# Kernel optimization log

Hardware: AMD Instinct MI355X
Metric: run time of the kernel (lower is better)

Reference implementation:

```python
import jax, jax.numpy as jnp
import numpy as np

N = 100000
E = 1600000
C = 32          # in_channels
H = 256         # hidden_size


def setup_inputs() -> dict:
    key = jax.random.key(0)
    ks = jax.random.split(key, 16)
    s = 1.0 / np.sqrt(C)
    inp = {
        "state": jax.random.normal(ks[0], (N, C), dtype=jnp.float32),
        "edge_index": jax.random.randint(ks[1], (2, E), 0, N, dtype=jnp.int64),
        # GCNConv params (conv3 reused for layers 4 and 5, matching the source)
        "convW1": jax.random.normal(ks[2], (C, C), dtype=jnp.float32) * s,
        "convb1": jnp.zeros((C,), jnp.float32),
        "convW2": jax.random.normal(ks[3], (C, C), dtype=jnp.float32) * s,
        "convb2": jnp.zeros((C,), jnp.float32),
        "convW3": jax.random.normal(ks[4], (C, C), dtype=jnp.float32) * s,
        "convb3": jnp.zeros((C,), jnp.float32),
        "linW1": jax.random.normal(ks[5], (6 * C, H), dtype=jnp.float32) / np.sqrt(6 * C),
        "linb1": jnp.zeros((H,), jnp.float32),
        "linW2": jax.random.normal(ks[6], (H, H), dtype=jnp.float32) / np.sqrt(H),
        "linb2": jnp.zeros((H,), jnp.float32),
        "linW3": jax.random.normal(ks[7], (H, 1), dtype=jnp.float32) / np.sqrt(H),
        "linb3": jnp.zeros((1,), jnp.float32),
    }
    return inp


def _gcn(x, W, b, src, dst, norm):
    # PyG GCNConv: x' = scatter_add( norm * (xW)[src] -> dst ) + b
    xw = x @ W                                  # [N, C]
    msg = norm[:, None] * xw[src]               # [E+N, C] gather
    agg = jax.ops.segment_sum(msg, dst, num_segments=x.shape[0])
    return agg + b


def reference(state, edge_index, convW1, convb1, convW2, convb2, convW3, convb3,
              linW1, linb1, linW2, linb2, linW3, linb3):
    n = state.shape[0]
    loops = jnp.arange(n, dtype=edge_index.dtype)
    src = jnp.concatenate([edge_index[0], loops])   # add self loops
    dst = jnp.concatenate([edge_index[1], loops])
    deg = jax.ops.segment_sum(jnp.ones_like(dst, dtype=state.dtype), dst, num_segments=n)
    dinv = jnp.where(deg > 0, jax.lax.rsqrt(deg), 0.0)
    norm = dinv[src] * dinv[dst]                    # symmetric normalization

    out1 = jax.nn.relu(_gcn(state, convW1, convb1, src, dst, norm))
    out2 = jax.nn.relu(_gcn(out1, convW2, convb2, src, dst, norm))
    out3 = jax.nn.relu(_gcn(out2, convW3, convb3, src, dst, norm))
    out4 = jax.nn.relu(_gcn(out3, convW3, convb3, src, dst, norm))  # conv3 reused (as in source)
    out5 = jax.nn.relu(_gcn(out4, convW3, convb3, src, dst, norm))  # conv3 reused (as in source)

    x = jnp.concatenate([out1, out2, out3, out4, out5, state], axis=-1)  # [N, 6C]
    x = jax.nn.leaky_relu(x @ linW1 + linb1, negative_slope=0.01)
    x = jax.nn.leaky_relu(x @ linW2 + linb2, negative_slope=0.01)
    x = jax.nn.softplus(x @ linW3 + linb3)
    concentration = jnp.squeeze(x, -1)              # [N]
    # deterministic=True path
    action = concentration / (concentration.sum(axis=-1, keepdims=True) + 1e-20)
    return action
```

## Files before the change

### kernel.cpp

```cpp
#include <hip/hip_runtime.h>
#include <hip/hip_bf16.h>
#include <hip/hip_fp16.h>

#define CDIV(a,b) (((a)+(b)-1)/(b))

typedef float f32x4 __attribute__((ext_vector_type(4)));
typedef int   i32x4 __attribute__((ext_vector_type(4)));
typedef unsigned int u32x2 __attribute__((ext_vector_type(2)));

__device__ __forceinline__ void mfma16(f32x4& d, i32x4 a, i32x4 b) {
  asm("v_mfma_f32_16x16x32_bf16 %0, %1, %2, %0" : "+v"(d) : "v"(a), "v"(b));
}

__device__ __forceinline__ unsigned short bf16r(float x) {
  return __builtin_bit_cast(unsigned short, __float2bfloat16(x));
}
__device__ __forceinline__ float bf16f(unsigned short u) {
  unsigned int w_ = (unsigned int)u << 16;
  return __builtin_bit_cast(float, w_);
}


__global__ __launch_bounds__(256) void k_count(const int* __restrict__ dst,
                                               int* __restrict__ cnt, int E) {
  int e = blockIdx.x * blockDim.x + threadIdx.x;
  if (e < E) atomicAdd(&cnt[dst[e]], 1);
}

__global__ __launch_bounds__(256) void k_scan1(const int* __restrict__ cnt,
                                               int* __restrict__ rowptr,
                                               int* __restrict__ blockSums, int N) {
  __shared__ int sdata[256];
  const int t = threadIdx.x;
  const int base = blockIdx.x * 1024;
  int v[4]; int local = 0;
#pragma unroll
  for (int i = 0; i < 4; i++) {
    int idx = base + t * 4 + i;
    v[i] = (idx < N) ? cnt[idx] : 0;
    local += v[i];
  }
  sdata[t] = local;
  __syncthreads();
  for (int off = 1; off < 256; off <<= 1) {
    int x = (t >= off) ? sdata[t - off] : 0;
    __syncthreads();
    sdata[t] += x;
    __syncthreads();
  }
  if (t == 255) blockSums[blockIdx.x] = sdata[255];
  int run = sdata[t] - local;
#pragma unroll
  for (int i = 0; i < 4; i++) {
    int idx = base + t * 4 + i;
    if (idx < N) rowptr[idx] = run;
    run += v[i];
  }
}

__global__ __launch_bounds__(256) void k_scan2(int* blockSums, int NB) {
  __shared__ int sdata[256];
  int t = threadIdx.x;
  int v = (t < NB) ? blockSums[t] : 0;
  sdata[t] = v;
  __syncthreads();
  for (int off = 1; off < 256; off <<= 1) {
    int x = (t >= off) ? sdata[t - off] : 0;
    __syncthreads();
    sdata[t] += x;
    __syncthreads();
  }
  if (t < NB) blockSums[t] = sdata[t] - v;
}

__global__ __launch_bounds__(256) void k_scan3(int* __restrict__ rowptr,
                                               const int* __restrict__ blockSums,
                                               int N, int E) {
  int idx = blockIdx.x * blockDim.x + threadIdx.x;
  if (idx < N) rowptr[idx] += blockSums[idx >> 10];
  if (idx == 0) rowptr[N] = E;
}

__global__ __launch_bounds__(256) void k_fill(const int* __restrict__ src,
                                              const int* __restrict__ dst,
                                              const int* __restrict__ rowptr,
                                              int* __restrict__ cursor,
                                              int* __restrict__ colidx, int E) {
  int e = blockIdx.x * blockDim.x + threadIdx.x;
  if (e < E) {
    int d = dst[e];
    int pos = rowptr[d] + atomicAdd(&cursor[d], 1);
    colidx[pos] = src[e];
  }
}

__global__ __launch_bounds__(256) void k_dinv(const int* __restrict__ cnt,
                                              float* __restrict__ dinv, int N) {
  int i = blockIdx.x * blockDim.x + threadIdx.x;
  if (i < N) dinv[i] = rsqrtf((float)cnt[i] + 1.0f);
}

__global__ __launch_bounds__(256) void k_xw(const float* __restrict__ x,
                                            const float* __restrict__ W,
                                            const float* __restrict__ dinv,
                                            unsigned short* __restrict__ y, int N) {
  __shared__ float Ws[1024];
  int t = threadIdx.x;
#pragma unroll
  for (int i = 0; i < 4; i++) Ws[t + i * 256] = W[t + i * 256];
  __syncthreads();
  int gid = blockIdx.x * blockDim.x + t;
  int n = gid >> 4, c = (gid & 15) * 2;
  if (n < N) {
    const float4* xr4 = (const float4*)(x + (size_t)n * 32);
    float a0 = 0.f, a1 = 0.f;
#pragma unroll
    for (int k4 = 0; k4 < 8; k4++) {
      float4 xv = xr4[k4];
      int k = k4 * 4;
      a0 = fmaf(xv.x, Ws[(k + 0) * 32 + c], a0); a1 = fmaf(xv.x, Ws[(k + 0) * 32 + c + 1], a1);
      a0 = fmaf(xv.y, Ws[(k + 1) * 32 + c], a0); a1 = fmaf(xv.y, Ws[(k + 1) * 32 + c + 1], a1);
      a0 = fmaf(xv.z, Ws[(k + 2) * 32 + c], a0); a1 = fmaf(xv.z, Ws[(k + 2) * 32 + c + 1], a1);
      a0 = fmaf(xv.w, Ws[(k + 3) * 32 + c], a0); a1 = fmaf(xv.w, Ws[(k + 3) * 32 + c + 1], a1);
    }
    float dn = dinv[n];
    __half2 h = __floats2half2_rn(a0 * dn, a1 * dn);
    *(__half2*)&y[(size_t)gid * 2] = h;
  }
}

__device__ __forceinline__ void acc8(float* acc, uint4 v) {
  float2 f;
  f = __half22float2(__builtin_bit_cast(__half2, v.x)); acc[0] += f.x; acc[1] += f.y;
  f = __half22float2(__builtin_bit_cast(__half2, v.y)); acc[2] += f.x; acc[3] += f.y;
  f = __half22float2(__builtin_bit_cast(__half2, v.z)); acc[4] += f.x; acc[5] += f.y;
  f = __half22float2(__builtin_bit_cast(__half2, v.w)); acc[6] += f.x; acc[7] += f.y;
}

__global__ __launch_bounds__(256) void k_agg(const unsigned short* __restrict__ y,
                                             const int* __restrict__ rowptr,
                                             const int* __restrict__ colidx,
                                             const float* __restrict__ dinv,
                                             const float* __restrict__ b,
                                             float* __restrict__ out, int N) {
  int t = threadIdx.x;
  int q = t & 3;
  int n = blockIdx.x * 64 + (t >> 2);
  if (n >= N) return;
  const uint4* yrow = (const uint4*)y;
  float acc[8];
  {
    uint4 v = yrow[(size_t)n * 4 + q];
    float2 f;
    f = __half22float2(__builtin_bit_cast(__half2, v.x)); acc[0] = f.x; acc[1] = f.y;
    f = __half22float2(__builtin_bit_cast(__half2, v.y)); acc[2] = f.x; acc[3] = f.y;
    f = __half22float2(__builtin_bit_cast(__half2, v.z)); acc[4] = f.x; acc[5] = f.y;
    f = __half22float2(__builtin_bit_cast(__half2, v.w)); acc[6] = f.x; acc[7] = f.y;
  }
  int beg = rowptr[n], end = rowptr[n + 1];
  int j = beg;
  for (; j + 16 <= end; j += 16) {
    uint4 v[16];
#pragma unroll
    for (int u = 0; u < 16; u++) v[u] = yrow[(size_t)colidx[j + u] * 4 + q];
#pragma unroll
    for (int u = 0; u < 16; u++) acc8(acc, v[u]);
  }
  for (; j + 8 <= end; j += 8) {
    uint4 v[8];
#pragma unroll
    for (int u = 0; u < 8; u++) v[u] = yrow[(size_t)colidx[j + u] * 4 + q];
#pragma unroll
    for (int u = 0; u < 8; u++) acc8(acc, v[u]);
  }
  for (; j + 4 <= end; j += 4) {
    uint4 v[4];
#pragma unroll
    for (int u = 0; u < 4; u++) v[u] = yrow[(size_t)colidx[j + u] * 4 + q];
#pragma unroll
    for (int u = 0; u < 4; u++) acc8(acc, v[u]);
  }
  for (; j < end; j++) {
    uint4 v = yrow[(size_t)colidx[j] * 4 + q];
    acc8(acc, v);
  }
  float dn = dinv[n];
  int cb = q * 8;
  float4 r0, r1;
  r0.x = fmaxf(fmaf(dn, acc[0], b[cb + 0]), 0.f);
  r0.y = fmaxf(fmaf(dn, acc[1], b[cb + 1]), 0.f);
  r0.z = fmaxf(fmaf(dn, acc[2], b[cb + 2]), 0.f);
  r0.w = fmaxf(fmaf(dn, acc[3], b[cb + 3]), 0.f);
  r1.x = fmaxf(fmaf(dn, acc[4], b[cb + 4]), 0.f);
  r1.y = fmaxf(fmaf(dn, acc[5], b[cb + 5]), 0.f);
  r1.z = fmaxf(fmaf(dn, acc[6], b[cb + 6]), 0.f);
  r1.w = fmaxf(fmaf(dn, acc[7], b[cb + 7]), 0.f);
  ((float4*)out)[(size_t)n * 8 + q * 2 + 0] = r0;
  ((float4*)out)[(size_t)n * 8 + q * 2 + 1] = r1;
}

__global__ __launch_bounds__(256) void k_prepw(const float* __restrict__ W1,
                                               const float* __restrict__ W2,
                                               unsigned short* __restrict__ Wt1h,
                                               unsigned short* __restrict__ Wt1l,
                                               unsigned short* __restrict__ Wt2h,
                                               unsigned short* __restrict__ Wt2l) {
  int o = blockIdx.x * blockDim.x + threadIdx.x;
  if (o < 256 * 192) {
    int col = o / 192, k = o % 192;
    float v = W1[k * 256 + col];
    unsigned short h = bf16r(v);
    Wt1h[o] = h;
    Wt1l[o] = bf16r(v - bf16f(h));
  } else if (o < 256 * 192 + 256 * 256) {
    int o2 = o - 256 * 192;
    int col = o2 / 256, k = o2 % 256;
    float v = W2[k * 256 + col];
    unsigned short h = bf16r(v);
    Wt2h[o2] = h;
    Wt2l[o2] = bf16r(v - bf16f(h));
  }
}

__device__ __forceinline__ float softplusf(float x) {
  return fmaxf(x, 0.f) + log1pf(expf(-fabsf(x)));
}

#define XS_STRIDE 200
#define H1_STRIDE 264
#define MNODES 64

__global__ __launch_bounds__(512, 4) void k_mlp_mfma(
    const float* __restrict__ o1, const float* __restrict__ o2,
    const float* __restrict__ o3, const float* __restrict__ o4,
    const float* __restrict__ o5, const float* __restrict__ st,
    const unsigned short* __restrict__ Wt1h, const unsigned short* __restrict__ Wt1l,
    const float* __restrict__ b1,
    const unsigned short* __restrict__ Wt2h, const unsigned short* __restrict__ Wt2l,
    const float* __restrict__ b2,
    const float* __restrict__ W3, const float* __restrict__ b3,
    float* __restrict__ conc, int N) {
  __shared__ unsigned short smem[2 * MNODES * XS_STRIDE];
  __shared__ float red[8][MNODES];
  unsigned short* xsh = smem;
  unsigned short* xsl = smem + MNODES * XS_STRIDE;
  unsigned short* h1h = smem;

  const int t = threadIdx.x;
  const int w = t >> 6;
  const int l = t & 63;
  const int l15 = l & 15, lq = l >> 4;
  const int nodeBase = blockIdx.x * MNODES;

  const float* srcs[6] = {o1, o2, o3, o4, o5, st};
  for (int i = t; i < MNODES * 96; i += 512) {
    int n = i / 96, cp = (i % 96) * 2;
    int gn = nodeBase + n;
    unsigned int pkh = 0, pkl = 0;
    if (gn < N) {
      const float* s = srcs[cp >> 5] + (size_t)gn * 32 + (cp & 31);
      float2 v = *(const float2*)s;
      unsigned short h0 = bf16r(v.x), h1_ = bf16r(v.y);
      unsigned short l0 = bf16r(v.x - bf16f(h0)), l1 = bf16r(v.y - bf16f(h1_));
      pkh = ((unsigned)h1_ << 16) | h0;
      pkl = ((unsigned)l1 << 16) | l0;
    }
    *(unsigned int*)&xsh[n * XS_STRIDE + cp] = pkh;
    *(unsigned int*)&xsl[n * XS_STRIDE + cp] = pkl;
  }
  __syncthreads();

  const int ocBase = w * 32;

  f32x4 acc[2][4];
#pragma unroll
  for (int rt = 0; rt < 2; rt++)
#pragma unroll
    for (int nt = 0; nt < 4; nt++) acc[rt][nt] = (f32x4)0.f;

  for (int kt = 0; kt < 6; kt++) {
    i32x4 ah[2], al[2];
#pragma unroll
    for (int rt = 0; rt < 2; rt++) {
      size_t aoff = (size_t)(ocBase + rt * 16 + l15) * 192 + kt * 32 + lq * 8;
      ah[rt] = *(const i32x4*)&Wt1h[aoff];
      al[rt] = *(const i32x4*)&Wt1l[aoff];
    }
#pragma unroll
    for (int nt = 0; nt < 4; nt++) {
      int boff = (nt * 16 + l15) * XS_STRIDE + kt * 32 + lq * 8;
      i32x4 bh = *(const i32x4*)&xsh[boff];
      i32x4 bl = *(const i32x4*)&xsl[boff];
#pragma unroll
      for (int rt = 0; rt < 2; rt++) mfma16(acc[rt][nt], ah[rt], bh);
#pragma unroll
      for (int rt = 0; rt < 2; rt++) mfma16(acc[rt][nt], al[rt], bh);
#pragma unroll
      for (int rt = 0; rt < 2; rt++) mfma16(acc[rt][nt], ah[rt], bl);
    }
  }
  __syncthreads();

#pragma unroll
  for (int rt = 0; rt < 2; rt++) {
    const int oc0 = ocBase + rt * 16 + lq * 4;
    float bb0 = b1[oc0], bb1 = b1[oc0 + 1], bb2 = b1[oc0 + 2], bb3 = b1[oc0 + 3];
#pragma unroll
    for (int nt = 0; nt < 4; nt++) {
      float v0 = acc[rt][nt][0] + bb0; v0 = (v0 > 0.f) ? v0 : 0.01f * v0;
      float v1 = acc[rt][nt][1] + bb1; v1 = (v1 > 0.f) ? v1 : 0.01f * v1;
      float v2 = acc[rt][nt][2] + bb2; v2 = (v2 > 0.f) ? v2 : 0.01f * v2;
      float v3 = acc[rt][nt][3] + bb3; v3 = (v3 > 0.f) ? v3 : 0.01f * v3;
      u32x2 pkh;
      pkh[0] = ((unsigned)bf16r(v1) << 16) | bf16r(v0);
      pkh[1] = ((unsigned)bf16r(v3) << 16) | bf16r(v2);
      int row = nt * 16 + l15;
      *(u32x2*)&h1h[row * H1_STRIDE + oc0] = pkh;
    }
  }
  __syncthreads();

  f32x4 acc2[2][4];
#pragma unroll
  for (int rt = 0; rt < 2; rt++)
#pragma unroll
    for (int nt = 0; nt < 4; nt++) acc2[rt][nt] = (f32x4)0.f;

  for (int kt = 0; kt < 8; kt++) {
    i32x4 ah[2], al[2];
#pragma unroll
    for (int rt = 0; rt < 2; rt++) {
      size_t aoff = (size_t)(ocBase + rt * 16 + l15) * 256 + kt * 32 + lq * 8;
      ah[rt] = *(const i32x4*)&Wt2h[aoff];
      al[rt] = *(const i32x4*)&Wt2l[aoff];
    }
#pragma unroll
    for (int nt = 0; nt < 4; nt++) {
      int boff = (nt * 16 + l15) * H1_STRIDE + kt * 32 + lq * 8;
      i32x4 bh = *(const i32x4*)&h1h[boff];
#pragma unroll
      for (int rt = 0; rt < 2; rt++) mfma16(acc2[rt][nt], ah[rt], bh);
#pragma unroll
      for (int rt = 0; rt < 2; rt++) mfma16(acc2[rt][nt], al[rt], bh);
    }
  }

#pragma unroll
  for (int nt = 0; nt < 4; nt++) {
    float p = 0.f;
#pragma unroll
    for (int rt = 0; rt < 2; rt++) {
      const int oc0 = ocBase + rt * 16 + lq * 4;
#pragma unroll
      for (int j = 0; j < 4; j++) {
        float v = acc2[rt][nt][j] + b2[oc0 + j];
        v = (v > 0.f) ? v : 0.01f * v;
        p = fmaf(v, W3[oc0 + j], p);
      }
    }
    p += __shfl_xor(p, 16, 64);
    p += __shfl_xor(p, 32, 64);
    if (lq == 0) red[w][nt * 16 + l15] = p;
  }
  __syncthreads();

  if (t < MNODES) {
    int gn = nodeBase + t;
    if (gn < N) {
      float s = red[0][t] + red[1][t] + red[2][t] + red[3][t]
              + red[4][t] + red[5][t] + red[6][t] + red[7][t] + b3[0];
      conc[gn] = softplusf(s);
    }
  }
}

__global__ __launch_bounds__(256) void k_redsum(const float* __restrict__ conc,
                                                float* __restrict__ total, int N) {
  float s = 0.f;
  for (int i = blockIdx.x * blockDim.x + threadIdx.x; i < N; i += gridDim.x * blockDim.x)
    s += conc[i];
#pragma unroll
  for (int off = 32; off > 0; off >>= 1) s += __shfl_down(s, off, 64);
  __shared__ float ws_[4];
  if ((threadIdx.x & 63) == 0) ws_[threadIdx.x >> 6] = s;
  __syncthreads();
  if (threadIdx.x == 0) atomicAdd(total, ws_[0] + ws_[1] + ws_[2] + ws_[3]);
}

__global__ __launch_bounds__(256) void k_div(const float* __restrict__ conc,
                                             const float* __restrict__ total,
                                             float* __restrict__ out, int N) {
  int i = blockIdx.x * blockDim.x + threadIdx.x;
  if (i < N) out[i] = conc[i] / (total[0] + 1e-20f);
}

extern "C" void kernel_launch(void* const* d_in, const int* in_sizes, int n_in,
                              void* d_out, int out_size, void* d_ws, size_t ws_size,
                              hipStream_t stream) {
  const float* state = (const float*)d_in[0];
  const int*   ei    = (const int*)d_in[1];
  const float* cW1 = (const float*)d_in[2];
  const float* cb1 = (const float*)d_in[3];
  const float* cW2 = (const float*)d_in[4];
  const float* cb2 = (const float*)d_in[5];
  const float* cW3 = (const float*)d_in[6];
  const float* cb3 = (const float*)d_in[7];
  const float* lW1 = (const float*)d_in[8];
  const float* lb1 = (const float*)d_in[9];
  const float* lW2 = (const float*)d_in[10];
  const float* lb2 = (const float*)d_in[11];
  const float* lW3 = (const float*)d_in[12];
  const float* lb3 = (const float*)d_in[13];

  const int N = in_sizes[0] / 32;
  const int E = in_sizes[1] / 2;
  const int* srcI = ei;
  const int* dstI = ei + E;

  char* w = (char*)d_ws;
  size_t off = 0;
  auto alloc = [&](size_t bytes) -> void* {
    void* p = w + off;
    off = (off + bytes + 255) & ~(size_t)255;
    return p;
  };
  int*   cnt       = (int*)alloc((size_t)N * 4);
  int*   cursor    = (int*)alloc((size_t)N * 4);
  float* total     = (float*)alloc(256);
  size_t zbytes = off;
  int*   rowptr    = (int*)alloc(((size_t)N + 1) * 4);
  int*   blockSums = (int*)alloc(256 * 4);
  int*   colidx    = (int*)alloc((size_t)E * 4);
  float* dinv      = (float*)alloc((size_t)N * 4);
  unsigned short* ybuf = (unsigned short*)alloc((size_t)N * 32 * 2);
  float* out1      = (float*)alloc((size_t)N * 32 * 4);
  float* out2      = (float*)alloc((size_t)N * 32 * 4);
  float* out3      = (float*)alloc((size_t)N * 32 * 4);
  float* out4      = (float*)alloc((size_t)N * 32 * 4);
  float* out5      = (float*)alloc((size_t)N * 32 * 4);
  float* conc      = (float*)alloc((size_t)N * 4);
  unsigned short* Wt1h = (unsigned short*)alloc(256 * 192 * 2);
  unsigned short* Wt1l = (unsigned short*)alloc(256 * 192 * 2);
  unsigned short* Wt2h = (unsigned short*)alloc(256 * 256 * 2);
  unsigned short* Wt2l = (unsigned short*)alloc(256 * 256 * 2);

  const int TB = 256;
  hipMemsetAsync(d_ws, 0, zbytes, stream);

  k_count<<<CDIV(E, TB), TB, 0, stream>>>(dstI, cnt, E);
  int NB = CDIV(N, 1024);
  k_scan1<<<NB, TB, 0, stream>>>(cnt, rowptr, blockSums, N);
  k_scan2<<<1, TB, 0, stream>>>(blockSums, NB);
  k_scan3<<<CDIV(N, TB), TB, 0, stream>>>(rowptr, blockSums, N, E);
  k_fill<<<CDIV(E, TB), TB, 0, stream>>>(srcI, dstI, rowptr, cursor, colidx, E);
  k_dinv<<<CDIV(N, TB), TB, 0, stream>>>(cnt, dinv, N);
  k_prepw<<<CDIV(256 * 192 + 256 * 256, TB), TB, 0, stream>>>(lW1, lW2, Wt1h, Wt1l, Wt2h, Wt2l);

  struct Layer { const float* x; const float* W; const float* b; float* out; };
  Layer L[5] = {{state, cW1, cb1, out1},
                {out1,  cW2, cb2, out2},
                {out2,  cW3, cb3, out3},
                {out3,  cW3, cb3, out4},
                {out4,  cW3, cb3, out5}};
  for (int i = 0; i < 5; i++) {
    k_xw<<<CDIV(N * 16, TB), TB, 0, stream>>>(L[i].x, L[i].W, dinv, ybuf, N);
    k_agg<<<CDIV(N, 64), TB, 0, stream>>>(ybuf, rowptr, colidx, dinv, L[i].b, L[i].out, N);
  }

  k_mlp_mfma<<<CDIV(N, MNODES), 512, 0, stream>>>(out1, out2, out3, out4, out5, state,
                                                  Wt1h, Wt1l, lb1, Wt2h, Wt2l, lb2,
                                                  lW3, lb3, conc, N);
  k_redsum<<<256, TB, 0, stream>>>(conc, total, N);
  k_div<<<CDIV(N, TB), TB, 0, stream>>>(conc, total, (float*)d_out, N);
}
```

Baseline: 454.3 us.

## Sort nodes by degree for load-balanced aggregation

Builds a node permutation grouped by in-degree with a counting sort (histogram, scan and scatter kernels). The aggregation kernel then processes nodes in that order, so nodes sharing a wavefront have similar degrees, which is meant to reduce divergence and tail imbalance. The cost is three extra setup kernels, one extra indirection per node, and scattered writes to the output rows. With uniformly random edges the degree spread is narrow, so the benefit may be small.

```diff
diff --git a/kernel.cpp b/kernel.cpp
--- a/kernel.cpp
+++ b/kernel.cpp
@@ -100,6 +100,39 @@
   if (i < N) dinv[i] = rsqrtf((float)cnt[i] + 1.0f);
 }
 
+__global__ __launch_bounds__(256) void k_dhist(const int* __restrict__ cnt,
+                                               int* __restrict__ dbin, int N) {
+  int i = blockIdx.x * blockDim.x + threadIdx.x;
+  if (i < N) atomicAdd(&dbin[min(cnt[i], 511)], 1);
+}
+
+__global__ __launch_bounds__(512) void k_dscan(const int* __restrict__ dbin,
+                                               int* __restrict__ dbase) {
+  __shared__ int s[512];
+  int t = threadIdx.x;
+  int v = dbin[t];
+  s[t] = v;
+  __syncthreads();
+  for (int off = 1; off < 512; off <<= 1) {
+    int x = (t >= off) ? s[t - off] : 0;
+    __syncthreads();
+    s[t] += x;
+    __syncthreads();
+  }
+  dbase[t] = s[t] - v;
+}
+
+__global__ __launch_bounds__(256) void k_dscatter(const int* __restrict__ cnt,
+                                                  const int* __restrict__ dbase,
+                                                  int* __restrict__ dcur,
+                                                  int* __restrict__ perm, int N) {
+  int i = blockIdx.x * blockDim.x + threadIdx.x;
+  if (i < N) {
+    int d = min(cnt[i], 511);
+    perm[dbase[d] + atomicAdd(&dcur[d], 1)] = i;
+  }
+}
+
 __global__ __launch_bounds__(256) void k_xw(const float* __restrict__ x,
                                             const float* __restrict__ W,
                                             const float* __restrict__ dinv,
@@ -142,11 +175,13 @@
                                              const int* __restrict__ colidx,
                                              const float* __restrict__ dinv,
                                              const float* __restrict__ b,
+                                             const int* __restrict__ perm,
                                              float* __restrict__ out, int N) {
   int t = threadIdx.x;
   int q = t & 3;
-  int n = blockIdx.x * 64 + (t >> 2);
-  if (n >= N) return;
+  int idx = blockIdx.x * 64 + (t >> 2);
+  if (idx >= N) return;
+  int n = perm[idx];
   const uint4* yrow = (const uint4*)y;
   float acc[8];
   {
@@ -427,7 +462,11 @@
   int*   cnt       = (int*)alloc((size_t)N * 4);
   int*   cursor    = (int*)alloc((size_t)N * 4);
   float* total     = (float*)alloc(256);
+  int*   dbin      = (int*)alloc(512 * 4);
+  int*   dcur      = (int*)alloc(512 * 4);
   size_t zbytes = off;
+  int*   dbase     = (int*)alloc(512 * 4);
+  int*   perm      = (int*)alloc((size_t)N * 4);
   int*   rowptr    = (int*)alloc(((size_t)N + 1) * 4);
   int*   blockSums = (int*)alloc(256 * 4);
   int*   colidx    = (int*)alloc((size_t)E * 4);
@@ -454,6 +493,9 @@
   k_scan3<<<CDIV(N, TB), TB, 0, stream>>>(rowptr, blockSums, N, E);
   k_fill<<<CDIV(E, TB), TB, 0, stream>>>(srcI, dstI, rowptr, cursor, colidx, E);
   k_dinv<<<CDIV(N, TB), TB, 0, stream>>>(cnt, dinv, N);
+  k_dhist<<<CDIV(N, TB), TB, 0, stream>>>(cnt, dbin, N);
+  k_dscan<<<1, 512, 0, stream>>>(dbin, dbase);
+  k_dscatter<<<CDIV(N, TB), TB, 0, stream>>>(cnt, dbase, dcur, perm, N);
   k_prepw<<<CDIV(256 * 192 + 256 * 256, TB), TB, 0, stream>>>(lW1, lW2, Wt1h, Wt1l, Wt2h, Wt2l);
 
   struct Layer { const float* x; const float* W; const float* b; float* out; };
@@ -464,7 +506,7 @@
                 {out4,  cW3, cb3, out5}};
   for (int i = 0; i < 5; i++) {
     k_xw<<<CDIV(N * 16, TB), TB, 0, stream>>>(L[i].x, L[i].W, dinv, ybuf, N);
-    k_agg<<<CDIV(N, 64), TB, 0, stream>>>(ybuf, rowptr, colidx, dinv, L[i].b, L[i].out, N);
+    k_agg<<<CDIV(N, 64), TB, 0, stream>>>(ybuf, rowptr, colidx, dinv, L[i].b, perm, L[i].out, N);
   }
 
   k_mlp_mfma<<<CDIV(N, MNODES), 512, 0, stream>>>(out1, out2, out3, out4, out5, state,
```

After: 1.014 ms. +123.3%, slower.
